# Kernel tuning notes

Hardware: AMD Instinct MI355X
Metric: run time of the kernel (lower is better)

Reference implementation:

```python
import jax, jax.numpy as jnp
import numpy as np

TOP_K = 2

def setup_inputs() -> dict:
    key = jax.random.key(0)
    ks = jax.random.split(key, 5)
    B, T, D, F, E = 4, 2048, 1024, 4096, 8
    s = 0.02
    return {
        "x": jax.random.normal(ks[0], (B, T, D), jnp.float32),
        "gate_w": jax.random.normal(ks[1], (D, E), jnp.float32) * s,
        "w1": jax.random.normal(ks[2], (E, D, F), jnp.float32) * s,
        "w3": jax.random.normal(ks[3], (E, D, F), jnp.float32) * s,
        "w2": jax.random.normal(ks[4], (E, F, D), jnp.float32) * s,
    }

def reference(x, gate_w, w1, w3, w2):
    # Router: logits -> softmax -> top-k -> renormalize (eval mode: no jitter)
    logits = jnp.einsum("btd,de->bte", x, gate_w)          # (B,T,E)
    probs = jax.nn.softmax(logits, axis=-1)
    expert_weights, expert_indices = jax.lax.top_k(probs, TOP_K)  # (B,T,K)
    expert_weights = expert_weights / expert_weights.sum(-1, keepdims=True)

    E = w1.shape[0]
    out = jnp.zeros_like(x)
    # Loop over small fixed expert count; per-token weight is 0 for non-routed
    # tokens, so dense compute + weighted sum matches the masked gather/scatter.
    for i in range(E):
        wi = jnp.where(expert_indices == i, expert_weights, 0.0).sum(-1)  # (B,T)
        h = jax.nn.silu(jnp.einsum("btd,df->btf", x, w1[i])) \
            * jnp.einsum("btd,df->btf", x, w3[i])                         # SwiGLU
        out = out + jnp.einsum("btf,fd->btd", h, w2[i]) * wi[..., None]
    return out
```

## Files before the change

### kernel.cpp

```cpp
#include <hip/hip_runtime.h>
#include <hip/hip_bf16.h>


#define NTOK 8192
#define DMODEL 1024
#define FDIM 4096
#define NEXP 8

typedef __attribute__((ext_vector_type(8))) short s8v;
typedef __attribute__((ext_vector_type(4))) float f4v;

__device__ __forceinline__ int imin(int a, int b){ return a < b ? a : b; }

__device__ __forceinline__ unsigned short f2b(float f){
  union { float f; unsigned u; } v; v.f = f;
  unsigned r = v.u + 0x7fffu + ((v.u >> 16) & 1u);
  return (unsigned short)(r >> 16);
}

__device__ __forceinline__ f4v mfma16(s8v a, s8v b, f4v c){
  return __builtin_amdgcn_mfma_f32_16x16x32_bf16(a, b, c, 0, 0, 0);
}

#define GLDS16(gp, lp) __builtin_amdgcn_global_load_lds(                      \
    (const __attribute__((address_space(1))) void*)(gp),                      \
    (__attribute__((address_space(3))) void*)(lp), 16, 0, 0)


__global__ void k_cvt(const float4* __restrict__ in, ushort4* __restrict__ out, int n4){
  int i = blockIdx.x * blockDim.x + threadIdx.x;
  int st = gridDim.x * blockDim.x;
  for(; i < n4; i += st){
    float4 v = in[i];
    ushort4 o;
    o.x = f2b(v.x); o.y = f2b(v.y); o.z = f2b(v.z); o.w = f2b(v.w);
    out[i] = o;
  }
}

__global__ void k_tr(const float* __restrict__ in, unsigned short* __restrict__ out,
                     int R, int C){
  __shared__ float tile[32][33];
  const float* src = in + (size_t)blockIdx.z * R * C;
  unsigned short* dst = out + (size_t)blockIdx.z * R * C;
  int bx = blockIdx.x * 32, by = blockIdx.y * 32;
  int tx = threadIdx.x & 31, ty = threadIdx.x >> 5;
  #pragma unroll
  for(int i = 0; i < 32; i += 8)
    tile[ty + i][tx] = src[(size_t)(by + ty + i) * C + bx + tx];
  __syncthreads();
  #pragma unroll
  for(int i = 0; i < 32; i += 8)
    dst[(size_t)(bx + ty + i) * R + by + tx] = f2b(tile[tx][ty + i]);
}

__global__ void k_router(const float* __restrict__ x, const float* __restrict__ gw,
                         int* __restrict__ route_e, float* __restrict__ route_w,
                         int* __restrict__ counts){
  int lane = threadIdx.x & 63;
  int t = blockIdx.x * 4 + (threadIdx.x >> 6);
  const float* xr = x + (size_t)t * DMODEL;
  float acc[NEXP];
  #pragma unroll
  for(int e = 0; e < NEXP; e++) acc[e] = 0.f;
  for(int d = lane; d < DMODEL; d += 64){
    float xv = xr[d];
    const float* g = gw + d * NEXP;
    #pragma unroll
    for(int e = 0; e < NEXP; e++) acc[e] += xv * g[e];
  }
  #pragma unroll
  for(int off = 32; off > 0; off >>= 1){
    #pragma unroll
    for(int e = 0; e < NEXP; e++) acc[e] += __shfl_down(acc[e], off, 64);
  }
  if(lane == 0){
    float mx = acc[0];
    #pragma unroll
    for(int e = 1; e < NEXP; e++) mx = fmaxf(mx, acc[e]);
    float p[NEXP];
    #pragma unroll
    for(int e = 0; e < NEXP; e++) p[e] = expf(acc[e] - mx);
    int i0 = 0;
    #pragma unroll
    for(int e = 1; e < NEXP; e++) if(p[e] > p[i0]) i0 = e;
    int i1 = (i0 == 0) ? 1 : 0;
    #pragma unroll
    for(int e = 0; e < NEXP; e++) if(e != i0 && p[e] > p[i1]) i1 = e;
    float inv = 1.f / (p[i0] + p[i1]);
    route_e[2*t]   = i0; route_e[2*t+1] = i1;
    route_w[2*t]   = p[i0] * inv;
    route_w[2*t+1] = p[i1] * inv;
    atomicAdd(&counts[i0], 1); atomicAdd(&counts[i1], 1);
  }
}

__global__ void k_scan(const int* __restrict__ counts, int* __restrict__ offsets,
                       int* __restrict__ cursor){
  if(threadIdx.x == 0){
    int o = 0;
    for(int e = 0; e < NEXP; e++){ offsets[e] = o; o += counts[e]; cursor[e] = 0; }
    offsets[NEXP] = o;
  }
}

__global__ void k_fill(const int* __restrict__ route_e, const float* __restrict__ route_w,
                       const int* __restrict__ offsets, int* __restrict__ cursor,
                       int* __restrict__ pair_tok, float* __restrict__ pair_wt,
                       int* __restrict__ t2p){
  int t = blockIdx.x * blockDim.x + threadIdx.x;
  if(t >= NTOK) return;
  #pragma unroll
  for(int k = 0; k < 2; k++){
    int e = route_e[2*t + k];
    int pos = atomicAdd(&cursor[e], 1);
    int gidx = offsets[e] + pos;
    pair_tok[gidx] = t;
    pair_wt[gidx] = route_w[2*t + k];
    t2p[2*t + k] = gidx;
  }
}

__global__ __launch_bounds__(256, 2) void k_ffn1(
    const unsigned short* __restrict__ xb,
    const unsigned short* __restrict__ w1t,
    const unsigned short* __restrict__ w3t,
    const int* __restrict__ counts, const int* __restrict__ offsets,
    const int* __restrict__ pair_tok,
    unsigned short* __restrict__ h)
{
  int e = blockIdx.z;
  int cnt = counts[e];
  int m0 = blockIdx.x * 128;
  if(m0 >= cnt) return;
  int off = offsets[e];
  int n0 = blockIdx.y * 128;

  __shared__ short As[2][128*32];
  __shared__ short B1s[2][128*32];
  __shared__ short B3s[2][128*32];
  __shared__ int stok[128];

  int tid = threadIdx.x;
  if(tid < 128){
    int pr = m0 + tid;
    stok[tid] = pair_tok[off + imin(pr, cnt - 1)];
  }
  __syncthreads();

  int wave = tid >> 6, lane = tid & 63;
  int rr  = wave * 32 + (lane >> 2);
  int g16 = (((lane & 3) ^ ((lane >> 3) & 3))) * 16;
  int wo = wave * 32 * 32;

  const char* a0 = (const char*)xb + (size_t)stok[rr]      * (DMODEL*2) + g16;
  const char* a1 = (const char*)xb + (size_t)stok[rr + 16] * (DMODEL*2) + g16;
  const char* b1base = (const char*)w1t + ((size_t)e * FDIM + n0) * (DMODEL*2);
  const char* b3base = (const char*)w3t + ((size_t)e * FDIM + n0) * (DMODEL*2);
  const char* b1_0 = b1base + (size_t)rr * (DMODEL*2) + g16;
  const char* b1_1 = b1_0 + (size_t)16 * (DMODEL*2);
  const char* b3_0 = b3base + (size_t)rr * (DMODEL*2) + g16;
  const char* b3_1 = b3_0 + (size_t)16 * (DMODEL*2);

  f4v zero = {0.f, 0.f, 0.f, 0.f};
  f4v acc1[4][4], acc3[4][4];
  #pragma unroll
  for(int i = 0; i < 4; i++)
    #pragma unroll
    for(int j = 0; j < 4; j++){ acc1[i][j] = zero; acc3[i][j] = zero; }

  int wm = wave & 1, wn = wave >> 1;
  int lm = lane & 15, quad = lane >> 4;
  int rp = (quad ^ ((lm >> 1) & 3)) * 8;

  GLDS16(a0,   As[0]  + wo); GLDS16(a1,   As[0]  + wo + 512);
  GLDS16(b1_0, B1s[0] + wo); GLDS16(b1_1, B1s[0] + wo + 512);
  GLDS16(b3_0, B3s[0] + wo); GLDS16(b3_1, B3s[0] + wo + 512);
  __syncthreads();

  for(int kt = 0; kt < DMODEL; kt += 32){
    int c = (kt >> 5) & 1;
    if(kt + 32 < DMODEL){
      int kb = (kt + 32) * 2;
      short* an  = As[c^1]  + wo;
      short* b1n = B1s[c^1] + wo;
      short* b3n = B3s[c^1] + wo;
      GLDS16(a0   + kb, an);  GLDS16(a1   + kb, an  + 512);
      GLDS16(b1_0 + kb, b1n); GLDS16(b1_1 + kb, b1n + 512);
      GLDS16(b3_0 + kb, b3n); GLDS16(b3_1 + kb, b3n + 512);
    }

    const short* Ab  = As[c];
    const short* B1b = B1s[c];
    const short* B3b = B3s[c];
    s8v af[4], b1f[4], b3f[4];
    #pragma unroll
    for(int mi = 0; mi < 4; mi++)
      af[mi] = *(const s8v*)(Ab + (wm*64 + mi*16 + lm)*32 + rp);
    #pragma unroll
    for(int ni = 0; ni < 4; ni++){
      b1f[ni] = *(const s8v*)(B1b + (wn*64 + ni*16 + lm)*32 + rp);
      b3f[ni] = *(const s8v*)(B3b + (wn*64 + ni*16 + lm)*32 + rp);
    }
    #pragma unroll
    for(int mi = 0; mi < 4; mi++)
      #pragma unroll
      for(int ni = 0; ni < 4; ni++){
        acc1[mi][ni] = mfma16(af[mi], b1f[ni], acc1[mi][ni]);
        acc3[mi][ni] = mfma16(af[mi], b3f[ni], acc3[mi][ni]);
      }
    __syncthreads();
  }

  #pragma unroll
  for(int mi = 0; mi < 4; mi++){
    int prb = m0 + wm*64 + mi*16 + quad*4;
    #pragma unroll
    for(int i = 0; i < 4; i++){
      int pr = prb + i;
      if(pr < cnt){
        size_t hrow = (size_t)(off + pr) * FDIM + n0 + wn*64 + lm;
        #pragma unroll
        for(int ni = 0; ni < 4; ni++){
          float p = acc1[mi][ni][i];
          float q = acc3[mi][ni][i];
          float hv = (p / (1.f + __expf(-p))) * q;
          h[hrow + ni*16] = f2b(hv);
        }
      }
    }
  }
}

__global__ __launch_bounds__(256, 2) void k_ffn2(
    const unsigned short* __restrict__ h,
    const unsigned short* __restrict__ w2t,
    const int* __restrict__ counts, const int* __restrict__ offsets,
    const float* __restrict__ pair_wt,
    float* __restrict__ pout)
{
  int e = blockIdx.z;
  int cnt = counts[e];
  int m0 = blockIdx.x * 128;
  if(m0 >= cnt) return;
  int off = offsets[e];
  int n0 = blockIdx.y * 128;

  __shared__ short As[2][128*32];
  __shared__ short Bs[2][128*32];

  int tid = threadIdx.x, wave = tid >> 6, lane = tid & 63;
  int rr  = wave * 32 + (lane >> 2);
  int g16 = (((lane & 3) ^ ((lane >> 3) & 3))) * 16;
  int wo = wave * 32 * 32;

  int pr0 = imin(m0 + rr,      cnt - 1);
  int pr1 = imin(m0 + rr + 16, cnt - 1);
  const char* a0 = (const char*)h + (size_t)(off + pr0) * (FDIM*2) + g16;
  const char* a1 = (const char*)h + (size_t)(off + pr1) * (FDIM*2) + g16;
  const char* bbase = (const char*)w2t + ((size_t)e * DMODEL + n0) * (FDIM*2);
  const char* b0 = bbase + (size_t)rr * (FDIM*2) + g16;
  const char* b1p = b0 + (size_t)16 * (FDIM*2);

  f4v zero = {0.f, 0.f, 0.f, 0.f};
  f4v acc[4][4];
  #pragma unroll
  for(int i = 0; i < 4; i++)
    #pragma unroll
    for(int j = 0; j < 4; j++) acc[i][j] = zero;

  int wm = wave & 1, wn = wave >> 1;
  int lm = lane & 15, quad = lane >> 4;
  int rp = (quad ^ ((lm >> 1) & 3)) * 8;

  GLDS16(a0, As[0] + wo); GLDS16(a1,  As[0] + wo + 512);
  GLDS16(b0, Bs[0] + wo); GLDS16(b1p, Bs[0] + wo + 512);
  __syncthreads();

  for(int kt = 0; kt < FDIM; kt += 32){
    int c = (kt >> 5) & 1;
    if(kt + 32 < FDIM){
      int kb = (kt + 32) * 2;
      short* an = As[c^1] + wo;
      short* bn = Bs[c^1] + wo;
      GLDS16(a0  + kb, an); GLDS16(a1  + kb, an + 512);
      GLDS16(b0  + kb, bn); GLDS16(b1p + kb, bn + 512);
    }

    const short* Ab = As[c];
    const short* Bb = Bs[c];
    s8v af[4], bf[4];
    #pragma unroll
    for(int mi = 0; mi < 4; mi++)
      af[mi] = *(const s8v*)(Ab + (wm*64 + mi*16 + lm)*32 + rp);
    #pragma unroll
    for(int ni = 0; ni < 4; ni++)
      bf[ni] = *(const s8v*)(Bb + (wn*64 + ni*16 + lm)*32 + rp);
    #pragma unroll
    for(int mi = 0; mi < 4; mi++)
      #pragma unroll
      for(int ni = 0; ni < 4; ni++)
        acc[mi][ni] = mfma16(af[mi], bf[ni], acc[mi][ni]);
    __syncthreads();
  }

  #pragma unroll
  for(int mi = 0; mi < 4; mi++){
    int prb = m0 + wm*64 + mi*16 + quad*4;
    #pragma unroll
    for(int i = 0; i < 4; i++){
      int pr = prb + i;
      if(pr < cnt){
        int gp = off + pr;
        float wt = pair_wt[gp];
        float* prow = pout + (size_t)gp * DMODEL + n0 + wn*64 + lm;
        #pragma unroll
        for(int ni = 0; ni < 4; ni++)
          prow[ni*16] = acc[mi][ni][i] * wt;
      }
    }
  }
}

__global__ void k_combine(const float4* __restrict__ pout, const int* __restrict__ t2p,
                          float4* __restrict__ out){
  int t = blockIdx.x;
  int d = threadIdx.x;
  int p0 = t2p[2*t], p1 = t2p[2*t + 1];
  out[(size_t)t * 256 + d] = pout[(size_t)p0 * 256 + d] + pout[(size_t)p1 * 256 + d];
}

extern "C" void kernel_launch(void* const* d_in, const int* in_sizes, int n_in,
                              void* d_out, int out_size, void* d_ws, size_t ws_size,
                              hipStream_t stream){
  const float* x  = (const float*)d_in[0];
  const float* gw = (const float*)d_in[1];
  const float* w1 = (const float*)d_in[2];
  const float* w3 = (const float*)d_in[3];
  const float* w2 = (const float*)d_in[4];
  float* out = (float*)d_out;

  char* ws = (char*)d_ws;
  size_t o = 0;
  auto alloc = [&](size_t b){ size_t r = o; o += (b + 255) & ~(size_t)255; return r; };
  unsigned short* xb  = (unsigned short*)(ws + alloc((size_t)NTOK * DMODEL * 2));
  unsigned short* w1t = (unsigned short*)(ws + alloc((size_t)NEXP * DMODEL * FDIM * 2));
  unsigned short* w3t = (unsigned short*)(ws + alloc((size_t)NEXP * DMODEL * FDIM * 2));
  unsigned short* w2t = (unsigned short*)(ws + alloc((size_t)NEXP * DMODEL * FDIM * 2));
  unsigned short* h   = (unsigned short*)(ws + alloc((size_t)2 * NTOK * FDIM * 2));
  int*   route_e  = (int*)  (ws + alloc(2 * NTOK * 4));
  float* route_w  = (float*)(ws + alloc(2 * NTOK * 4));
  int*   counts   = (int*)  (ws + alloc(256));
  int*   offsets  = (int*)  (ws + alloc(256));
  int*   cursor   = (int*)  (ws + alloc(256));
  int*   pair_tok = (int*)  (ws + alloc(2 * NTOK * 4));
  float* pair_wt  = (float*)(ws + alloc(2 * NTOK * 4));
  int*   t2p      = (int*)  (ws + alloc(2 * NTOK * 4));
  float* pout = (float*)w1t;

  hipMemsetAsync(counts, 0, 256, stream);

  k_cvt<<<2048, 256, 0, stream>>>((const float4*)x, (ushort4*)xb, NTOK * DMODEL / 4);
  k_tr<<<dim3(FDIM/32, DMODEL/32, NEXP), 256, 0, stream>>>(w1, w1t, DMODEL, FDIM);
  k_tr<<<dim3(FDIM/32, DMODEL/32, NEXP), 256, 0, stream>>>(w3, w3t, DMODEL, FDIM);
  k_tr<<<dim3(DMODEL/32, FDIM/32, NEXP), 256, 0, stream>>>(w2, w2t, FDIM, DMODEL);

  k_router<<<NTOK/4, 256, 0, stream>>>(x, gw, route_e, route_w, counts);
  k_scan<<<1, 64, 0, stream>>>(counts, offsets, cursor);
  k_fill<<<NTOK/256, 256, 0, stream>>>(route_e, route_w, offsets, cursor, pair_tok, pair_wt, t2p);

  k_ffn1<<<dim3(64, FDIM/128, NEXP), 256, 0, stream>>>(xb, w1t, w3t, counts, offsets, pair_tok, h);
  k_ffn2<<<dim3(64, DMODEL/128, NEXP), 256, 0, stream>>>(h, w2t, counts, offsets, pair_wt, pout);
  k_combine<<<NTOK, 256, 0, stream>>>((const float4*)pout, t2p, (float4*)out);
}
```

Baseline: 1.630 ms.

## Triple-buffer LDS pipeline with vmcnt waits and expert-interleaved block swizzle in FFN kernels

```diff
diff --git a/kernel.cpp b/kernel.cpp
--- a/kernel.cpp
+++ b/kernel.cpp
@@ -129,16 +129,21 @@
     const int* __restrict__ pair_tok,
     unsigned short* __restrict__ h)
 {
-  int e = blockIdx.z;
+  unsigned lin = blockIdx.x + ((blockIdx.y + (blockIdx.z << 5)) << 6);
+  unsigned swz = ((lin & 7u) << 11) | (lin >> 3);
+  int e  = swz >> 11;
+  int bx = swz & 63;
+  int by = (swz >> 6) & 31;
+
   int cnt = counts[e];
-  int m0 = blockIdx.x * 128;
+  int m0 = bx * 128;
   if(m0 >= cnt) return;
   int off = offsets[e];
-  int n0 = blockIdx.y * 128;
-
-  __shared__ short As[2][128*32];
-  __shared__ short B1s[2][128*32];
-  __shared__ short B3s[2][128*32];
+  int n0 = by * 128;
+
+  __shared__ short As[3][128*32];
+  __shared__ short B1s[3][128*32];
+  __shared__ short B3s[3][128*32];
   __shared__ int stok[128];
 
   int tid = threadIdx.x;
@@ -162,6 +167,16 @@
   const char* b3_0 = b3base + (size_t)rr * (DMODEL*2) + g16;
   const char* b3_1 = b3_0 + (size_t)16 * (DMODEL*2);
 
+  auto stage = [&](int tt, int buf){
+    int kb = tt << 6;
+    short* an  = &As[buf][wo];
+    short* b1n = &B1s[buf][wo];
+    short* b3n = &B3s[buf][wo];
+    GLDS16(a0   + kb, an);  GLDS16(a1   + kb, an  + 512);
+    GLDS16(b1_0 + kb, b1n); GLDS16(b1_1 + kb, b1n + 512);
+    GLDS16(b3_0 + kb, b3n); GLDS16(b3_1 + kb, b3n + 512);
+  };
+
   f4v zero = {0.f, 0.f, 0.f, 0.f};
   f4v acc1[4][4], acc3[4][4];
   #pragma unroll
@@ -173,26 +188,21 @@
   int lm = lane & 15, quad = lane >> 4;
   int rp = (quad ^ ((lm >> 1) & 3)) * 8;
 
-  GLDS16(a0,   As[0]  + wo); GLDS16(a1,   As[0]  + wo + 512);
-  GLDS16(b1_0, B1s[0] + wo); GLDS16(b1_1, B1s[0] + wo + 512);
-  GLDS16(b3_0, B3s[0] + wo); GLDS16(b3_1, B3s[0] + wo + 512);
-  __syncthreads();
-
-  for(int kt = 0; kt < DMODEL; kt += 32){
-    int c = (kt >> 5) & 1;
-    if(kt + 32 < DMODEL){
-      int kb = (kt + 32) * 2;
-      short* an  = As[c^1]  + wo;
-      short* b1n = B1s[c^1] + wo;
-      short* b3n = B3s[c^1] + wo;
-      GLDS16(a0   + kb, an);  GLDS16(a1   + kb, an  + 512);
-      GLDS16(b1_0 + kb, b1n); GLDS16(b1_1 + kb, b1n + 512);
-      GLDS16(b3_0 + kb, b3n); GLDS16(b3_1 + kb, b3n + 512);
+  stage(0, 0); stage(1, 1);
+  asm volatile("s_waitcnt vmcnt(6)" ::: "memory");
+  __builtin_amdgcn_s_barrier();
+
+  int bufc = 0;
+  for(int t = 0; t < 32; ++t){
+    int nb = t + 2;
+    if(nb < 32){
+      int bufn = bufc + 2; if(bufn >= 3) bufn -= 3;
+      stage(nb, bufn);
     }
 
-    const short* Ab  = As[c];
-    const short* B1b = B1s[c];
-    const short* B3b = B3s[c];
+    const short* Ab  = As[bufc];
+    const short* B1b = B1s[bufc];
+    const short* B3b = B3s[bufc];
     s8v af[4], b1f[4], b3f[4];
     #pragma unroll
     for(int mi = 0; mi < 4; mi++)
@@ -209,7 +219,11 @@
         acc1[mi][ni] = mfma16(af[mi], b1f[ni], acc1[mi][ni]);
         acc3[mi][ni] = mfma16(af[mi], b3f[ni], acc3[mi][ni]);
       }
-    __syncthreads();
+
+    if(nb < 32)      asm volatile("s_waitcnt vmcnt(6) lgkmcnt(0)" ::: "memory");
+    else if(t < 31)  asm volatile("s_waitcnt vmcnt(0) lgkmcnt(0)" ::: "memory");
+    if(t < 31) __builtin_amdgcn_s_barrier();
+    if(++bufc == 3) bufc = 0;
   }
 
   #pragma unroll
@@ -225,7 +239,7 @@
           float p = acc1[mi][ni][i];
           float q = acc3[mi][ni][i];
           float hv = (p / (1.f + __expf(-p))) * q;
-          h[hrow + ni*16] = f2b(hv);
+          __builtin_nontemporal_store((unsigned short)f2b(hv), &h[hrow + ni*16]);
         }
       }
     }
@@ -239,15 +253,20 @@
     const float* __restrict__ pair_wt,
     float* __restrict__ pout)
 {
-  int e = blockIdx.z;
+  unsigned lin = blockIdx.x + ((blockIdx.y + (blockIdx.z << 3)) << 6);
+  unsigned swz = ((lin & 7u) << 9) | (lin >> 3);
+  int e  = swz >> 9;
+  int bx = swz & 63;
+  int by = (swz >> 6) & 7;
+
   int cnt = counts[e];
-  int m0 = blockIdx.x * 128;
+  int m0 = bx * 128;
   if(m0 >= cnt) return;
   int off = offsets[e];
-  int n0 = blockIdx.y * 128;
-
-  __shared__ short As[2][128*32];
-  __shared__ short Bs[2][128*32];
+  int n0 = by * 128;
+
+  __shared__ short As[3][128*32];
+  __shared__ short Bs[3][128*32];
 
   int tid = threadIdx.x, wave = tid >> 6, lane = tid & 63;
   int rr  = wave * 32 + (lane >> 2);
@@ -262,6 +281,14 @@
   const char* b0 = bbase + (size_t)rr * (FDIM*2) + g16;
   const char* b1p = b0 + (size_t)16 * (FDIM*2);
 
+  auto stage = [&](int tt, int buf){
+    int kb = tt << 6;
+    short* an = &As[buf][wo];
+    short* bn = &Bs[buf][wo];
+    GLDS16(a0 + kb, an); GLDS16(a1  + kb, an + 512);
+    GLDS16(b0 + kb, bn); GLDS16(b1p + kb, bn + 512);
+  };
+
   f4v zero = {0.f, 0.f, 0.f, 0.f};
   f4v acc[4][4];
   #pragma unroll
@@ -273,22 +300,20 @@
   int lm = lane & 15, quad = lane >> 4;
   int rp = (quad ^ ((lm >> 1) & 3)) * 8;
 
-  GLDS16(a0, As[0] + wo); GLDS16(a1,  As[0] + wo + 512);
-  GLDS16(b0, Bs[0] + wo); GLDS16(b1p, Bs[0] + wo + 512);
-  __syncthreads();
-
-  for(int kt = 0; kt < FDIM; kt += 32){
-    int c = (kt >> 5) & 1;
-    if(kt + 32 < FDIM){
-      int kb = (kt + 32) * 2;
-      short* an = As[c^1] + wo;
-      short* bn = Bs[c^1] + wo;
-      GLDS16(a0  + kb, an); GLDS16(a1  + kb, an + 512);
-      GLDS16(b0  + kb, bn); GLDS16(b1p + kb, bn + 512);
+  stage(0, 0); stage(1, 1);
+  asm volatile("s_waitcnt vmcnt(4)" ::: "memory");
+  __builtin_amdgcn_s_barrier();
+
+  int bufc = 0;
+  for(int t = 0; t < 128; ++t){
+    int nb = t + 2;
+    if(nb < 128){
+      int bufn = bufc + 2; if(bufn >= 3) bufn -= 3;
+      stage(nb, bufn);
     }
 
-    const short* Ab = As[c];
-    const short* Bb = Bs[c];
+    const short* Ab = As[bufc];
+    const short* Bb = Bs[bufc];
     s8v af[4], bf[4];
     #pragma unroll
     for(int mi = 0; mi < 4; mi++)
@@ -301,7 +326,11 @@
       #pragma unroll
       for(int ni = 0; ni < 4; ni++)
         acc[mi][ni] = mfma16(af[mi], bf[ni], acc[mi][ni]);
-    __syncthreads();
+
+    if(nb < 128)      asm volatile("s_waitcnt vmcnt(4) lgkmcnt(0)" ::: "memory");
+    else if(t < 127)  asm volatile("s_waitcnt vmcnt(0) lgkmcnt(0)" ::: "memory");
+    if(t < 127) __builtin_amdgcn_s_barrier();
+    if(++bufc == 3) bufc = 0;
   }
 
   #pragma unroll
@@ -316,7 +345,7 @@
         float* prow = pout + (size_t)gp * DMODEL + n0 + wn*64 + lm;
         #pragma unroll
         for(int ni = 0; ni < 4; ni++)
-          prow[ni*16] = acc[mi][ni][i] * wt;
+          __builtin_nontemporal_store(acc[mi][ni][i] * wt, prow + ni*16);
       }
     }
   }
```

New measurement: 1.361 ms. 1.2x faster.
